# Optimization experiments

Hardware: AMD Instinct MI355X
Metric: run time of the kernel (lower is better)

The kernel has to match this reference:

```python
import jax, jax.numpy as jnp
import numpy as np

N = 8192      # number of graph nodes
C = 256       # feature_size
D = C // 2    # projection dim


def setup_inputs() -> dict:
    key = jax.random.key(0)
    ks = jax.random.split(key, 10)
    s_in = 1.0 / np.sqrt(C + 3)   # torch Linear default init scale (uniform bound)
    s_r = 1.0 / np.sqrt(D)
    return {
        "landmarks": jax.random.normal(ks[0], (1, N, 3), dtype=jnp.float32),
        "features": jax.random.normal(ks[1], (1, N, C), dtype=jnp.float32),
        # weights stored [in, out]
        "Wi": jax.random.uniform(ks[2], (C + 3, D), jnp.float32, -s_in, s_in),
        "bi": jax.random.uniform(ks[3], (D,), jnp.float32, -s_in, s_in),
        "Wj": jax.random.uniform(ks[4], (C + 3, D), jnp.float32, -s_in, s_in),
        "bj": jax.random.uniform(ks[5], (D,), jnp.float32, -s_in, s_in),
        "Wk": jax.random.uniform(ks[6], (C + 3, D), jnp.float32, -s_in, s_in),
        "bk": jax.random.uniform(ks[7], (D,), jnp.float32, -s_in, s_in),
        "Wr": jax.random.uniform(ks[8], (D, C), jnp.float32, -s_r, s_r),
        "br": jax.random.uniform(ks[9], (C,), jnp.float32, -s_r, s_r),
    }


def reference(landmarks, features, Wi, bi, Wj, bj, Wk, bk, Wr, br):
    # concat coords + features, drop the singleton batch dim: [N, C+3]
    x = jnp.concatenate([landmarks, features], axis=2)[0]
    fi = x @ Wi + bi                       # [N, D]
    fj = x @ Wj + bj                       # [N, D]
    fk = x @ Wk + bk                       # [N, D]
    att = jax.nn.sigmoid(fi @ fj.T)        # [N, N] sigmoid scores (non-softmax)
    att = att / jnp.sum(att, axis=1, keepdims=True)  # row-sum normalize
    out = (att @ fk) @ Wr + br             # [N, C] restored
    return features + out[None]            # residual, back to [1, N, C]
```

## Files before the change

kernel.cpp:

```cpp
#include <hip/hip_runtime.h>
#include <stdint.h>

#define N_NODES 8192
#define KPAD 272
#define OUTC 384

typedef __attribute__((ext_vector_type(8))) short bhalf8;
typedef __attribute__((ext_vector_type(16))) float f32x16;
typedef __attribute__((ext_vector_type(4))) float f32x4;

__device__ inline unsigned short f2bf_rne(float f) {
    unsigned u = __builtin_bit_cast(unsigned, f);
    u += 0x7FFFu + ((u >> 16) & 1u);
    return (unsigned short)(u >> 16);
}

__device__ inline bhalf8 mk8(unsigned a, unsigned b, unsigned c, unsigned d) {
    union { unsigned u[4]; bhalf8 v; } U;
    U.u[0] = a; U.u[1] = b; U.u[2] = c; U.u[3] = d;
    return U.v;
}

__device__ inline void pl32swap(unsigned& a, unsigned& b) {
    asm("v_permlane32_swap_b32 %0, %1" : "+v"(a), "+v"(b));
}

#define GLD_TO_LDS(gptr, lptr)                                                              \
    __builtin_amdgcn_global_load_lds((const __attribute__((address_space(1))) void*)(gptr), \
                                     (__attribute__((address_space(3))) void*)(lptr), 16, 0, 0)

__global__ void k_prep(const float* __restrict__ Wi, const float* __restrict__ bi,
                       const float* __restrict__ Wj, const float* __restrict__ bj,
                       const float* __restrict__ Wk, const float* __restrict__ bk,
                       const float* __restrict__ Wr,
                       unsigned short* __restrict__ WcatT, unsigned short* __restrict__ WrT,
                       float* __restrict__ bcat) {
    int idx = blockIdx.x * 256 + threadIdx.x;
    const int WC_N = OUTC * KPAD;
    const int WR_N = 256 * 128;
    if (idx < WC_N) {
        int n = idx / KPAD, kk = idx - n * KPAD;
        int sel = n >> 7, d = n & 127;
        const float* W = (sel == 0) ? Wi : ((sel == 1) ? Wj : Wk);
        float v = 0.f;
        if (kk < 256) v = W[(kk + 3) * 128 + d];
        else if (kk < 259) v = W[(kk - 256) * 128 + d];
        WcatT[idx] = f2bf_rne(v);
        return;
    }
    idx -= WC_N;
    if (idx < WR_N) {
        int c = idx >> 7, d = idx & 127;
        WrT[idx] = f2bf_rne(Wr[d * 256 + c]);
        return;
    }
    idx -= WR_N;
    if (idx < OUTC) {
        float v = (idx < 128) ? bi[idx] : ((idx < 256) ? bj[idx - 128] : bk[idx - 256]);
        bcat[idx] = v;
    }
}

__global__ __launch_bounds__(256) void k_proj(const float* __restrict__ landmarks,
                                              const float* __restrict__ features,
                                              const unsigned short* __restrict__ WcatT,
                                              const float* __restrict__ bcat,
                                              unsigned short* __restrict__ fi,
                                              unsigned short* __restrict__ fj,
                                              unsigned short* __restrict__ fkT) {
    const int tid = threadIdx.x, w = tid >> 6, l = tid & 63, h = l >> 5, ln = l & 31;
    const unsigned bid = blockIdx.x;
    const int it = bid / 3, ng = bid - it * 3;
    const int i0 = it * 32;
    const int n = ng * 128 + w * 32 + ln;
    const int row = i0 + ln;
    f32x16 acc = {};
#pragma unroll
    for (int s = 0; s < 17; ++s) {
        union { unsigned short us[8]; bhalf8 v; } A;
        if (s < 16) {
            const float* fp = features + (size_t)row * 256 + s * 16 + h * 8;
            f32x4 v0 = *(const f32x4*)(fp);
            f32x4 v1 = *(const f32x4*)(fp + 4);
#pragma unroll
            for (int e = 0; e < 4; ++e) { A.us[e] = f2bf_rne(v0[e]); A.us[4 + e] = f2bf_rne(v1[e]); }
        } else {
#pragma unroll
            for (int e = 0; e < 8; ++e) A.us[e] = 0;
            if (h == 0) {
                A.us[0] = f2bf_rne(landmarks[row * 3 + 0]);
                A.us[1] = f2bf_rne(landmarks[row * 3 + 1]);
                A.us[2] = f2bf_rne(landmarks[row * 3 + 2]);
            }
        }
        bhalf8 b = *(const bhalf8*)(WcatT + (size_t)n * KPAD + s * 16 + h * 8);
        acc = __builtin_amdgcn_mfma_f32_32x32x16_bf16(A.v, b, acc, 0, 0, 0);
    }
    const int d = w * 32 + ln;
    const float bias = bcat[n];
    if (ng < 2) {
        unsigned short* dst = ng ? fj : fi;
#pragma unroll
        for (int q = 0; q < 4; ++q) {
            int ib = i0 + 8 * q + 4 * h;
#pragma unroll
            for (int r = 0; r < 4; ++r)
                dst[(size_t)(ib + r) * 128 + d] = f2bf_rne(acc[4 * q + r] + bias);
        }
    } else {
#pragma unroll
        for (int q = 0; q < 4; ++q) {
            int ib = i0 + 8 * q + 4 * h;
            ushort4 pk;
            pk.x = f2bf_rne(acc[4 * q + 0] + bias);
            pk.y = f2bf_rne(acc[4 * q + 1] + bias);
            pk.z = f2bf_rne(acc[4 * q + 2] + bias);
            pk.w = f2bf_rne(acc[4 * q + 3] + bias);
            *(ushort4*)(fkT + (size_t)d * N_NODES + ib) = pk;
        }
    }
}

__global__ __launch_bounds__(256, 2) void k_attn(const unsigned short* __restrict__ fi,
                                                 const unsigned short* __restrict__ fj,
                                                 const unsigned short* __restrict__ fkT,
                                                 float* __restrict__ num_part,
                                                 float* __restrict__ den_part) {
    __shared__ __align__(16) char smem[65536];
    char* const fjb0 = smem;
    char* const fkb0 = smem + 16384;
    char* const fjb1 = smem + 32768;
    char* const fkb1 = smem + 49152;

    const int tid = threadIdx.x;
    const int w = tid >> 6, l = tid & 63, h = l >> 5, ln = l & 31;
    const int ih = w >> 1, jh = w & 1;
    const unsigned b = blockIdx.x;
    const int xcd = b & 7;
    const int jq = xcd >> 1;
    const int rt = (int)(b >> 3) + ((xcd & 1) << 6);
    const int i0 = rt * 64;
    const int jbase = jq * 2048;

    const int rsub = l >> 4, cph = l & 15;

    bhalf8 bfi[8];
#pragma unroll
    for (int s = 0; s < 8; ++s)
        bfi[s] = *(const bhalf8*)(fi + (size_t)(i0 + ih * 32 + ln) * 128 + s * 16 + h * 8);

    f32x16 acc[4] = {};
    float dacc = 0.f;

    auto STAGE = [&](char* fjd, char* fkd, int J0) {
#pragma unroll
        for (int q = 0; q < 4; ++q) {
            int r = w * 16 + q * 4 + rsub;
            int c = cph ^ (r & 15);
            GLD_TO_LDS(fj + (size_t)(J0 + r) * 128 + c * 8, fjd + (w * 16 + q * 4) * 256);
        }
#pragma unroll
        for (int q = 0; q < 4; ++q) {
            int r = w * 16 + q * 4 + rsub;
            int g = cph ^ (r & 15);
            int d = r + ((g >> 3) << 6);
            int joff = (g & 7) * 8;
            GLD_TO_LDS(fkT + (size_t)d * N_NODES + J0 + joff, fkd + (w * 16 + q * 4) * 256);
        }
    };

    auto COMPUTE = [&](const char* fjbuf, const char* fkbuf) {
        f32x16 sa = {}, sb = {};
        const int jrow = jh * 32 + ln;
        __builtin_amdgcn_s_setprio(1);
#pragma unroll
        for (int ss = 0; ss < 4; ++ss) {
            int se = 2 * ss, so = 2 * ss + 1;
            int ce = (se * 2 + h) ^ (jrow & 15);
            int co = (so * 2 + h) ^ (jrow & 15);
            bhalf8 ae = *(const bhalf8*)(fjbuf + jrow * 256 + ce * 16);
            bhalf8 ao = *(const bhalf8*)(fjbuf + jrow * 256 + co * 16);
            sa = __builtin_amdgcn_mfma_f32_32x32x16_bf16(ae, bfi[se], sa, 0, 0, 0);
            sb = __builtin_amdgcn_mfma_f32_32x32x16_bf16(ao, bfi[so], sb, 0, 0, 0);
        }
        __builtin_amdgcn_s_setprio(0);
        unsigned p[8];
#pragma unroll
        for (int q = 0; q < 8; ++q) {
            float e0 = sa[2 * q] + sb[2 * q];
            float e1 = sa[2 * q + 1] + sb[2 * q + 1];
            float x0 = __builtin_amdgcn_rcpf(1.f + __builtin_amdgcn_exp2f(e0 * -1.44269504f));
            float x1 = __builtin_amdgcn_rcpf(1.f + __builtin_amdgcn_exp2f(e1 * -1.44269504f));
            dacc += x0;
            dacc += x1;
            p[q] = __builtin_amdgcn_perm(__builtin_bit_cast(unsigned, x1),
                                         __builtin_bit_cast(unsigned, x0), 0x07060302u);
        }
        unsigned w0 = p[0], w2 = p[2]; pl32swap(w0, w2);
        unsigned w1 = p[1], w3 = p[3]; pl32swap(w1, w3);
        bhalf8 fb0 = mk8(w0, w1, w2, w3);
        __builtin_amdgcn_s_setprio(1);
#pragma unroll
        for (int m4 = 0; m4 < 4; ++m4) {
            int d = m4 * 32 + ln;
            int r = d & 63;
            int g = ((d >> 6) << 3) | (jh * 4 + h);
            int slot = g ^ (r & 15);
            bhalf8 af = *(const bhalf8*)(fkbuf + r * 256 + slot * 16);
            acc[m4] = __builtin_amdgcn_mfma_f32_32x32x16_bf16(af, fb0, acc[m4], 0, 0, 0);
        }
        unsigned w4 = p[4], w6 = p[6]; pl32swap(w4, w6);
        unsigned w5 = p[5], w7 = p[7]; pl32swap(w5, w7);
        bhalf8 fb1 = mk8(w4, w5, w6, w7);
#pragma unroll
        for (int m4 = 0; m4 < 4; ++m4) {
            int d = m4 * 32 + ln;
            int r = d & 63;
            int g = ((d >> 6) << 3) | (jh * 4 + 2 + h);
            int slot = g ^ (r & 15);
            bhalf8 af = *(const bhalf8*)(fkbuf + r * 256 + slot * 16);
            acc[m4] = __builtin_amdgcn_mfma_f32_32x32x16_bf16(af, fb1, acc[m4], 0, 0, 0);
        }
        __builtin_amdgcn_s_setprio(0);
    };

    STAGE(fjb0, fkb0, jbase);
    __syncthreads();
#pragma unroll 1
    for (int mt = 0; mt < 32; mt += 2) {
        STAGE(fjb1, fkb1, jbase + (mt + 1) * 64);
        COMPUTE(fjb0, fkb0);
        __syncthreads();
        if (mt + 2 < 32) STAGE(fjb0, fkb0, jbase + (mt + 2) * 64);
        COMPUTE(fjb1, fkb1);
        __syncthreads();
    }

    dacc += __shfl_xor(dacc, 32, 64);
    float* denb = (float*)(smem + 40960);
    if (h == 0) denb[w * 32 + ln] = dacc;

    float* buf = (float*)smem;
    if (jh == 0) {
#pragma unroll
        for (int m4 = 0; m4 < 4; ++m4)
#pragma unroll
            for (int q = 0; q < 4; ++q) {
                f32x4 v = {acc[m4][4 * q + 0], acc[m4][4 * q + 1],
                           acc[m4][4 * q + 2], acc[m4][4 * q + 3]};
                *(f32x4*)(buf + (ih * 32 + ln) * 132 + m4 * 32 + 8 * q + 4 * h) = v;
            }
    }
    __syncthreads();
    if (jh == 1) {
#pragma unroll
        for (int m4 = 0; m4 < 4; ++m4)
#pragma unroll
            for (int q = 0; q < 4; ++q) {
                float* p4 = buf + (ih * 32 + ln) * 132 + m4 * 32 + 8 * q + 4 * h;
                f32x4 old = *(f32x4*)p4;
                f32x4 v = {acc[m4][4 * q + 0], acc[m4][4 * q + 1],
                           acc[m4][4 * q + 2], acc[m4][4 * q + 3]};
                *(f32x4*)p4 = old + v;
            }
    }
    __syncthreads();
#pragma unroll
    for (int e = 0; e < 8; ++e) {
        int v = e * 256 + tid;
        int iloc = v >> 5, d4 = (v & 31) * 4;
        *(f32x4*)(num_part + ((size_t)jq * N_NODES + i0 + iloc) * 128 + d4) =
            *(const f32x4*)(buf + iloc * 132 + d4);
    }
    if (tid < 64) {
        den_part[(size_t)jq * N_NODES + i0 + tid] =
            denb[(tid >> 5) * 64 + (tid & 31)] + denb[(tid >> 5) * 64 + 32 + (tid & 31)];
    }
}

__global__ __launch_bounds__(256) void k_out(const unsigned short* __restrict__ WrT,
                                             const float* __restrict__ br,
                                             const float* __restrict__ features,
                                             const float* __restrict__ num_part,
                                             const float* __restrict__ den_part,
                                             float* __restrict__ out) {
    __shared__ __align__(16) char smem[73728];
    char* const tb = smem + 65536;
    const int tid = threadIdx.x, w = tid >> 6, l = tid & 63, h = l >> 5, ln = l & 31;
    const int i0 = blockIdx.x * 32;
    {
        int rsub = l >> 4, cph = l & 15;
#pragma unroll
        for (int q = 0; q < 16; ++q) {
            int r = w * 64 + q * 4 + rsub;
            int c = cph ^ (r & 15);
            GLD_TO_LDS(WrT + (size_t)r * 128 + c * 8, (char*)smem + (w * 64 + q * 4) * 256);
        }
    }
    {
        int i = tid >> 3, dseg = (tid & 7) * 16;
        f32x4 s[4] = {};
        float ds = 0.f;
#pragma unroll
        for (int q = 0; q < 4; ++q) {
            const float* np = num_part + ((size_t)(q * N_NODES + i0 + i)) * 128 + dseg;
#pragma unroll
            for (int k = 0; k < 4; ++k) s[k] += *(const f32x4*)(np + 4 * k);
            ds += den_part[(size_t)q * N_NODES + i0 + i];
        }
        float inv = 1.0f / ds;
#pragma unroll
        for (int cc = 0; cc < 2; ++cc) {
            union { unsigned u[4]; bhalf8 v; } U;
#pragma unroll
            for (int m = 0; m < 4; ++m) {
                int e0 = cc * 8 + 2 * m;
                unsigned lo = f2bf_rne(s[e0 >> 2][e0 & 3] * inv);
                unsigned hi = f2bf_rne(s[(e0 + 1) >> 2][(e0 + 1) & 3] * inv);
                U.u[m] = lo | (hi << 16);
            }
            int slot = ((tid & 7) * 2 + cc) ^ (i & 15);
            *(bhalf8*)(tb + i * 256 + slot * 16) = U.v;
        }
    }
    __syncthreads();
    f32x16 acc[2] = {};
#pragma unroll
    for (int s = 0; s < 8; ++s) {
        int ca = (s * 2 + h) ^ (ln & 15);
        bhalf8 af = *(const bhalf8*)(tb + ln * 256 + ca * 16);
#pragma unroll
        for (int nt = 0; nt < 2; ++nt) {
            int row = w * 64 + nt * 32 + ln;
            int c = (s * 2 + h) ^ (row & 15);
            bhalf8 bf = *(const bhalf8*)(smem + row * 256 + c * 16);
            acc[nt] = __builtin_amdgcn_mfma_f32_32x32x16_bf16(af, bf, acc[nt], 0, 0, 0);
        }
    }
#pragma unroll
    for (int nt = 0; nt < 2; ++nt) {
        int cc = w * 64 + nt * 32 + ln;
        float bias = br[cc];
#pragma unroll
        for (int q = 0; q < 4; ++q) {
#pragma unroll
            for (int r = 0; r < 4; ++r) {
                int i = i0 + 8 * q + 4 * h + r;
                out[(size_t)i * 256 + cc] = acc[nt][4 * q + r] + bias + features[(size_t)i * 256 + cc];
            }
        }
    }
}

extern "C" void kernel_launch(void* const* d_in, const int* in_sizes, int n_in,
                              void* d_out, int out_size, void* d_ws, size_t ws_size,
                              hipStream_t stream) {
    const float* landmarks = (const float*)d_in[0];
    const float* features  = (const float*)d_in[1];
    const float* Wi = (const float*)d_in[2];
    const float* bi = (const float*)d_in[3];
    const float* Wj = (const float*)d_in[4];
    const float* bj = (const float*)d_in[5];
    const float* Wk = (const float*)d_in[6];
    const float* bk = (const float*)d_in[7];
    const float* Wr = (const float*)d_in[8];
    const float* br = (const float*)d_in[9];

    char* ws = (char*)d_ws;
    unsigned short* WcatT   = (unsigned short*)(ws + 0);
    unsigned short* WrT     = (unsigned short*)(ws + 208896);
    float*          bcat    = (float*)(ws + 274432);
    unsigned short* fi      = (unsigned short*)(ws + 275968);
    unsigned short* fjp     = (unsigned short*)(ws + 2373120);
    unsigned short* fkT     = (unsigned short*)(ws + 4470272);
    float*          num_part= (float*)(ws + 6567424);
    float*          den_part= (float*)(ws + 23344640);

    float* out = (float*)d_out;

    hipLaunchKernelGGL(k_prep, dim3(538), dim3(256), 0, stream,
                       Wi, bi, Wj, bj, Wk, bk, Wr, WcatT, WrT, bcat);
    hipLaunchKernelGGL(k_proj, dim3(768), dim3(256), 0, stream,
                       landmarks, features, WcatT, bcat, fi, fjp, fkT);
    hipLaunchKernelGGL(k_attn, dim3(512), dim3(256), 0, stream, fi, fjp, fkT, num_part, den_part);
    hipLaunchKernelGGL(k_out, dim3(256), dim3(256), 0, stream,
                       WrT, br, features, num_part, den_part, out);
}
```

Measured before the change: 151.7 us.

## Software-pipeline QK MFMA of next tile with sigmoid and PV of previous

```diff
diff --git a/kernel.cpp b/kernel.cpp
--- a/kernel.cpp
+++ b/kernel.cpp
@@ -152,6 +152,10 @@
     f32x16 acc[4] = {};
     float dacc = 0.f;
 
+    f32x16 saA = {}, sbA = {}, saB = {}, sbB = {};
+    bhalf8 fkA[4], fkB[4];
+    bhalf8 fb0, fb1;
+
     auto STAGE = [&](char* fjd, char* fkd, int J0) {
 #pragma unroll
         for (int q = 0; q < 4; ++q) {
@@ -169,9 +173,9 @@
         }
     };
 
-    auto COMPUTE = [&](const char* fjbuf, const char* fkbuf) {
-        f32x16 sa = {}, sb = {};
+    auto QK = [&](const char* fjbuf, f32x16& sa, f32x16& sb) {
         const int jrow = jh * 32 + ln;
+        f32x16 ta = {}, tb = {};
         __builtin_amdgcn_s_setprio(1);
 #pragma unroll
         for (int ss = 0; ss < 4; ++ss) {
@@ -180,10 +184,14 @@
             int co = (so * 2 + h) ^ (jrow & 15);
             bhalf8 ae = *(const bhalf8*)(fjbuf + jrow * 256 + ce * 16);
             bhalf8 ao = *(const bhalf8*)(fjbuf + jrow * 256 + co * 16);
-            sa = __builtin_amdgcn_mfma_f32_32x32x16_bf16(ae, bfi[se], sa, 0, 0, 0);
-            sb = __builtin_amdgcn_mfma_f32_32x32x16_bf16(ao, bfi[so], sb, 0, 0, 0);
+            ta = __builtin_amdgcn_mfma_f32_32x32x16_bf16(ae, bfi[se], ta, 0, 0, 0);
+            tb = __builtin_amdgcn_mfma_f32_32x32x16_bf16(ao, bfi[so], tb, 0, 0, 0);
         }
         __builtin_amdgcn_s_setprio(0);
+        sa = ta; sb = tb;
+    };
+
+    auto SIG = [&](const f32x16& sa, const f32x16& sb) {
         unsigned p[8];
 #pragma unroll
         for (int q = 0; q < 8; ++q) {
@@ -198,43 +206,64 @@
         }
         unsigned w0 = p[0], w2 = p[2]; pl32swap(w0, w2);
         unsigned w1 = p[1], w3 = p[3]; pl32swap(w1, w3);
-        bhalf8 fb0 = mk8(w0, w1, w2, w3);
+        fb0 = mk8(w0, w1, w2, w3);
+        unsigned w4 = p[4], w6 = p[6]; pl32swap(w4, w6);
+        unsigned w5 = p[5], w7 = p[7]; pl32swap(w5, w7);
+        fb1 = mk8(w4, w5, w6, w7);
+    };
+
+    auto PV = [&]() {
         __builtin_amdgcn_s_setprio(1);
+#pragma unroll
+        for (int m4 = 0; m4 < 4; ++m4)
+            acc[m4] = __builtin_amdgcn_mfma_f32_32x32x16_bf16(fkA[m4], fb0, acc[m4], 0, 0, 0);
+#pragma unroll
+        for (int m4 = 0; m4 < 4; ++m4)
+            acc[m4] = __builtin_amdgcn_mfma_f32_32x32x16_bf16(fkB[m4], fb1, acc[m4], 0, 0, 0);
+        __builtin_amdgcn_s_setprio(0);
+    };
+
+    auto LOADFK = [&](const char* fkbuf) {
 #pragma unroll
         for (int m4 = 0; m4 < 4; ++m4) {
             int d = m4 * 32 + ln;
             int r = d & 63;
-            int g = ((d >> 6) << 3) | (jh * 4 + h);
-            int slot = g ^ (r & 15);
-            bhalf8 af = *(const bhalf8*)(fkbuf + r * 256 + slot * 16);
-            acc[m4] = __builtin_amdgcn_mfma_f32_32x32x16_bf16(af, fb0, acc[m4], 0, 0, 0);
-        }
-        unsigned w4 = p[4], w6 = p[6]; pl32swap(w4, w6);
-        unsigned w5 = p[5], w7 = p[7]; pl32swap(w5, w7);
-        bhalf8 fb1 = mk8(w4, w5, w6, w7);
-#pragma unroll
-        for (int m4 = 0; m4 < 4; ++m4) {
-            int d = m4 * 32 + ln;
-            int r = d & 63;
-            int g = ((d >> 6) << 3) | (jh * 4 + 2 + h);
-            int slot = g ^ (r & 15);
-            bhalf8 af = *(const bhalf8*)(fkbuf + r * 256 + slot * 16);
-            acc[m4] = __builtin_amdgcn_mfma_f32_32x32x16_bf16(af, fb1, acc[m4], 0, 0, 0);
-        }
-        __builtin_amdgcn_s_setprio(0);
+            int ghi = (d >> 6) << 3;
+            int gA = ghi | (jh * 4 + h);
+            int gB = ghi | (jh * 4 + 2 + h);
+            fkA[m4] = *(const bhalf8*)(fkbuf + r * 256 + (gA ^ (r & 15)) * 16);
+            fkB[m4] = *(const bhalf8*)(fkbuf + r * 256 + (gB ^ (r & 15)) * 16);
+        }
     };
 
     STAGE(fjb0, fkb0, jbase);
     __syncthreads();
+    STAGE(fjb1, fkb1, jbase + 64);
+    QK(fjb0, saA, sbA);
+    LOADFK(fkb0);
+    __syncthreads();
 #pragma unroll 1
-    for (int mt = 0; mt < 32; mt += 2) {
-        STAGE(fjb1, fkb1, jbase + (mt + 1) * 64);
-        COMPUTE(fjb0, fkb0);
+    for (int k = 1; k < 31; k += 2) {
+        STAGE(fjb0, fkb0, jbase + (k + 1) * 64);
+        QK(fjb1, saB, sbB);
+        SIG(saA, sbA);
+        PV();
+        LOADFK(fkb1);
         __syncthreads();
-        if (mt + 2 < 32) STAGE(fjb0, fkb0, jbase + (mt + 2) * 64);
-        COMPUTE(fjb1, fkb1);
+        if (k + 1 < 31) STAGE(fjb1, fkb1, jbase + (k + 2) * 64);
+        QK(fjb0, saA, sbA);
+        SIG(saB, sbB);
+        PV();
+        LOADFK(fkb0);
         __syncthreads();
     }
+    QK(fjb1, saB, sbB);
+    SIG(saA, sbA);
+    PV();
+    LOADFK(fkb1);
+    SIG(saB, sbB);
+    PV();
+    __syncthreads();
 
     dacc += __shfl_xor(dacc, 32, 64);
     float* denb = (float*)(smem + 40960);
```

Measured after the change: 152.8 us. No clear change (+0.7%).

## Load fj/fk fragments directly to registers via MFMA-ready global layouts

Applied to the files above, without the earlier changes.

```diff
diff --git a/kernel.cpp b/kernel.cpp
--- a/kernel.cpp
+++ b/kernel.cpp
@@ -66,8 +66,8 @@
                                               const unsigned short* __restrict__ WcatT,
                                               const float* __restrict__ bcat,
                                               unsigned short* __restrict__ fi,
-                                              unsigned short* __restrict__ fj,
-                                              unsigned short* __restrict__ fkT) {
+                                              unsigned short* __restrict__ fjF,
+                                              unsigned short* __restrict__ fkF) {
     const int tid = threadIdx.x, w = tid >> 6, l = tid & 63, h = l >> 5, ln = l & 31;
     const unsigned bid = blockIdx.x;
     const int it = bid / 3, ng = bid - it * 3;
@@ -98,14 +98,24 @@
     }
     const int d = w * 32 + ln;
     const float bias = bcat[n];
-    if (ng < 2) {
-        unsigned short* dst = ng ? fj : fi;
+    if (ng == 0) {
 #pragma unroll
         for (int q = 0; q < 4; ++q) {
             int ib = i0 + 8 * q + 4 * h;
 #pragma unroll
             for (int r = 0; r < 4; ++r)
-                dst[(size_t)(ib + r) * 128 + d] = f2bf_rne(acc[4 * q + r] + bias);
+                fi[(size_t)(ib + r) * 128 + d] = f2bf_rne(acc[4 * q + r] + bias);
+        }
+    } else if (ng == 1) {
+#pragma unroll
+        for (int q = 0; q < 4; ++q) {
+            int ib = i0 + 8 * q + 4 * h;
+#pragma unroll
+            for (int r = 0; r < 4; ++r) {
+                int j = ib + r;
+                fjF[(size_t)(j >> 6) * 8192 + (d >> 3) * 512 + (j & 63) * 8 + (d & 7)] =
+                    f2bf_rne(acc[4 * q + r] + bias);
+            }
         }
     } else {
 #pragma unroll
@@ -116,21 +126,17 @@
             pk.y = f2bf_rne(acc[4 * q + 1] + bias);
             pk.z = f2bf_rne(acc[4 * q + 2] + bias);
             pk.w = f2bf_rne(acc[4 * q + 3] + bias);
-            *(ushort4*)(fkT + (size_t)d * N_NODES + ib) = pk;
+            *(ushort4*)(fkF + (size_t)(ib >> 6) * 8192 + ((ib >> 3) & 7) * 1024 + d * 8 + 4 * h) = pk;
         }
     }
 }
 
 __global__ __launch_bounds__(256, 2) void k_attn(const unsigned short* __restrict__ fi,
-                                                 const unsigned short* __restrict__ fj,
-                                                 const unsigned short* __restrict__ fkT,
+                                                 const unsigned short* __restrict__ fjF,
+                                                 const unsigned short* __restrict__ fkF,
                                                  float* __restrict__ num_part,
                                                  float* __restrict__ den_part) {
-    __shared__ __align__(16) char smem[65536];
-    char* const fjb0 = smem;
-    char* const fkb0 = smem + 16384;
-    char* const fjb1 = smem + 32768;
-    char* const fkb1 = smem + 49152;
+    __shared__ __align__(16) char smem[36864];
 
     const int tid = threadIdx.x;
     const int w = tid >> 6, l = tid & 63, h = l >> 5, ln = l & 31;
@@ -140,9 +146,6 @@
     const int jq = xcd >> 1;
     const int rt = (int)(b >> 3) + ((xcd & 1) << 6);
     const int i0 = rt * 64;
-    const int jbase = jq * 2048;
-
-    const int rsub = l >> 4, cph = l & 15;
 
     bhalf8 bfi[8];
 #pragma unroll
@@ -152,38 +155,41 @@
     f32x16 acc[4] = {};
     float dacc = 0.f;
 
-    auto STAGE = [&](char* fjd, char* fkd, int J0) {
-#pragma unroll
-        for (int q = 0; q < 4; ++q) {
-            int r = w * 16 + q * 4 + rsub;
-            int c = cph ^ (r & 15);
-            GLD_TO_LDS(fj + (size_t)(J0 + r) * 128 + c * 8, fjd + (w * 16 + q * 4) * 256);
-        }
-#pragma unroll
-        for (int q = 0; q < 4; ++q) {
-            int r = w * 16 + q * 4 + rsub;
-            int g = cph ^ (r & 15);
-            int d = r + ((g >> 3) << 6);
-            int joff = (g & 7) * 8;
-            GLD_TO_LDS(fkT + (size_t)d * N_NODES + J0 + joff, fkd + (w * 16 + q * 4) * 256);
+    const unsigned short* fjp = fjF + (size_t)(jq * 32) * 8192 + (jh * 32 + ln) * 8 + h * 512;
+    const unsigned short* fkp = fkF + (size_t)(jq * 32) * 8192 + (jh * 4 + h) * 1024 + ln * 8;
+
+    bhalf8 fjc[8];
+    bhalf8 fkA[4], fkB[4];
+
+    auto LOADFJ = [&](const unsigned short* p) {
+#pragma unroll
+        for (int ss = 0; ss < 4; ++ss) {
+            fjc[2 * ss]     = *(const bhalf8*)(p + ss * 2048);
+            fjc[2 * ss + 1] = *(const bhalf8*)(p + ss * 2048 + 1024);
         }
     };
-
-    auto COMPUTE = [&](const char* fjbuf, const char* fkbuf) {
+    auto LOADFK = [&](const unsigned short* p) {
+#pragma unroll
+        for (int m4 = 0; m4 < 4; ++m4) {
+            fkA[m4] = *(const bhalf8*)(p + m4 * 256);
+            fkB[m4] = *(const bhalf8*)(p + 2048 + m4 * 256);
+        }
+    };
+
+    LOADFJ(fjp);
+    LOADFK(fkp);
+#pragma unroll 1
+    for (int mt = 0; mt < 32; ++mt) {
         f32x16 sa = {}, sb = {};
-        const int jrow = jh * 32 + ln;
         __builtin_amdgcn_s_setprio(1);
 #pragma unroll
         for (int ss = 0; ss < 4; ++ss) {
-            int se = 2 * ss, so = 2 * ss + 1;
-            int ce = (se * 2 + h) ^ (jrow & 15);
-            int co = (so * 2 + h) ^ (jrow & 15);
-            bhalf8 ae = *(const bhalf8*)(fjbuf + jrow * 256 + ce * 16);
-            bhalf8 ao = *(const bhalf8*)(fjbuf + jrow * 256 + co * 16);
-            sa = __builtin_amdgcn_mfma_f32_32x32x16_bf16(ae, bfi[se], sa, 0, 0, 0);
-            sb = __builtin_amdgcn_mfma_f32_32x32x16_bf16(ao, bfi[so], sb, 0, 0, 0);
+            sa = __builtin_amdgcn_mfma_f32_32x32x16_bf16(fjc[2 * ss], bfi[2 * ss], sa, 0, 0, 0);
+            sb = __builtin_amdgcn_mfma_f32_32x32x16_bf16(fjc[2 * ss + 1], bfi[2 * ss + 1], sb, 0, 0, 0);
         }
         __builtin_amdgcn_s_setprio(0);
+        fjp += 8192;
+        LOADFJ(fjp);
         unsigned p[8];
 #pragma unroll
         for (int q = 0; q < 8; ++q) {
@@ -199,48 +205,27 @@
         unsigned w0 = p[0], w2 = p[2]; pl32swap(w0, w2);
         unsigned w1 = p[1], w3 = p[3]; pl32swap(w1, w3);
         bhalf8 fb0 = mk8(w0, w1, w2, w3);
-        __builtin_amdgcn_s_setprio(1);
-#pragma unroll
-        for (int m4 = 0; m4 < 4; ++m4) {
-            int d = m4 * 32 + ln;
-            int r = d & 63;
-            int g = ((d >> 6) << 3) | (jh * 4 + h);
-            int slot = g ^ (r & 15);
-            bhalf8 af = *(const bhalf8*)(fkbuf + r * 256 + slot * 16);
-            acc[m4] = __builtin_amdgcn_mfma_f32_32x32x16_bf16(af, fb0, acc[m4], 0, 0, 0);
-        }
         unsigned w4 = p[4], w6 = p[6]; pl32swap(w4, w6);
         unsigned w5 = p[5], w7 = p[7]; pl32swap(w5, w7);
         bhalf8 fb1 = mk8(w4, w5, w6, w7);
-#pragma unroll
-        for (int m4 = 0; m4 < 4; ++m4) {
-            int d = m4 * 32 + ln;
-            int r = d & 63;
-            int g = ((d >> 6) << 3) | (jh * 4 + 2 + h);
-            int slot = g ^ (r & 15);
-            bhalf8 af = *(const bhalf8*)(fkbuf + r * 256 + slot * 16);
-            acc[m4] = __builtin_amdgcn_mfma_f32_32x32x16_bf16(af, fb1, acc[m4], 0, 0, 0);
-        }
+        __builtin_amdgcn_s_setprio(1);
+#pragma unroll
+        for (int m4 = 0; m4 < 4; ++m4)
+            acc[m4] = __builtin_amdgcn_mfma_f32_32x32x16_bf16(fkA[m4], fb0, acc[m4], 0, 0, 0);
+#pragma unroll
+        for (int m4 = 0; m4 < 4; ++m4)
+            acc[m4] = __builtin_amdgcn_mfma_f32_32x32x16_bf16(fkB[m4], fb1, acc[m4], 0, 0, 0);
         __builtin_amdgcn_s_setprio(0);
-    };
-
-    STAGE(fjb0, fkb0, jbase);
+        fkp += 8192;
+        LOADFK(fkp);
+    }
+
+    dacc += __shfl_xor(dacc, 32, 64);
+    float* denb = (float*)(smem + 34816);
+    if (h == 0) denb[w * 32 + ln] = dacc;
+
+    float* buf = (float*)smem;
     __syncthreads();
-#pragma unroll 1
-    for (int mt = 0; mt < 32; mt += 2) {
-        STAGE(fjb1, fkb1, jbase + (mt + 1) * 64);
-        COMPUTE(fjb0, fkb0);
-        __syncthreads();
-        if (mt + 2 < 32) STAGE(fjb0, fkb0, jbase + (mt + 2) * 64);
-        COMPUTE(fjb1, fkb1);
-        __syncthreads();
-    }
-
-    dacc += __shfl_xor(dacc, 32, 64);
-    float* denb = (float*)(smem + 40960);
-    if (h == 0) denb[w * 32 + ln] = dacc;
-
-    float* buf = (float*)smem;
     if (jh == 0) {
 #pragma unroll
         for (int m4 = 0; m4 < 4; ++m4)
@@ -371,8 +356,8 @@
     unsigned short* WrT     = (unsigned short*)(ws + 208896);
     float*          bcat    = (float*)(ws + 274432);
     unsigned short* fi      = (unsigned short*)(ws + 275968);
-    unsigned short* fjp     = (unsigned short*)(ws + 2373120);
-    unsigned short* fkT     = (unsigned short*)(ws + 4470272);
+    unsigned short* fjF     = (unsigned short*)(ws + 2373120);
+    unsigned short* fkF     = (unsigned short*)(ws + 4470272);
     float*          num_part= (float*)(ws + 6567424);
     float*          den_part= (float*)(ws + 23344640);
 
@@ -381,8 +366,8 @@
     hipLaunchKernelGGL(k_prep, dim3(538), dim3(256), 0, stream,
                        Wi, bi, Wj, bj, Wk, bk, Wr, WcatT, WrT, bcat);
     hipLaunchKernelGGL(k_proj, dim3(768), dim3(256), 0, stream,
-                       landmarks, features, WcatT, bcat, fi, fjp, fkT);
-    hipLaunchKernelGGL(k_attn, dim3(512), dim3(256), 0, stream, fi, fjp, fkT, num_part, den_part);
+                       landmarks, features, WcatT, bcat, fi, fjF, fkF);
+    hipLaunchKernelGGL(k_attn, dim3(512), dim3(256), 0, stream, fi, fjF, fkF, num_part, den_part);
     hipLaunchKernelGGL(k_out, dim3(256), dim3(256), 0, stream,
                        WrT, br, features, num_part, den_part, out);
 }
```

Result: no change. 151.0 us (-0.5%).
